# Kernel tuning notes

Hardware: AMD Instinct MI355X
Metric: run time of the kernel (lower is better)

Reference implementation:

```python
import jax, jax.numpy as jnp
import numpy as np
from jax import lax

D_MODEL = 512
EXPAND = 2
INNER = D_MODEL * EXPAND
K = 4
B, T = 8, 2048
LN_EPS = 1e-5


def setup_inputs() -> dict:
    key = jax.random.key(0)
    ks = jax.random.split(key, 12)
    s_in = 1.0 / np.sqrt(D_MODEL)
    s_out = 1.0 / np.sqrt(INNER)
    return {
        "x": jax.random.normal(ks[0], (B, T, D_MODEL), dtype=jnp.float32),
        "ln_w": jnp.ones((D_MODEL,), jnp.float32),
        "ln_b": jnp.zeros((D_MODEL,), jnp.float32),
        "in_proj_w": jax.random.uniform(ks[1], (3 * INNER, D_MODEL), jnp.float32, -s_in, s_in),
        "in_proj_b": jax.random.uniform(ks[2], (3 * INNER,), jnp.float32, -s_in, s_in),
        "conv_w": jax.random.uniform(ks[3], (INNER, 1, K), jnp.float32, -0.5, 0.5),
        "conv_b": jax.random.uniform(ks[4], (INNER,), jnp.float32, -0.5, 0.5),
        "delta_w": jax.random.uniform(ks[5], (INNER, D_MODEL), jnp.float32, -s_in, s_in),
        "delta_b": jax.random.uniform(ks[6], (INNER,), jnp.float32, -s_in, s_in),
        "state_mix": jnp.zeros((INNER,), jnp.float32),
        "skip_scale": jnp.ones((INNER,), jnp.float32),
        "out_proj_w": jax.random.uniform(ks[7], (D_MODEL, INNER), jnp.float32, -s_out, s_out),
        "out_proj_b": jax.random.uniform(ks[8], (D_MODEL,), jnp.float32, -s_out, s_out),
    }


def _layernorm(x, w, b):
    mu = jnp.mean(x, axis=-1, keepdims=True)
    var = jnp.mean(jnp.square(x - mu), axis=-1, keepdims=True)
    return (x - mu) * lax.rsqrt(var + LN_EPS) * w + b


def _causal_dw_conv(x_bct, w, b):
    # x: [B, C, T], w: [C, 1, K] depthwise, left pad K-1 (causal)
    y = lax.conv_general_dilated(
        x_bct, w, window_strides=(1,), padding=[(K - 1, 0)],
        dimension_numbers=("NCH", "OIH", "NCH"), feature_group_count=INNER)
    return y + b[None, :, None]


def reference(x, ln_w, ln_b, in_proj_w, in_proj_b, conv_w, conv_b,
              delta_w, delta_b, state_mix, skip_scale, out_proj_w, out_proj_b):
    residual = x
    xn = _layernorm(x, ln_w, ln_b)                      # [B,T,D]
    h = xn @ in_proj_w.T + in_proj_b                     # [B,T,3*INNER]
    proj, gate, drive = jnp.split(h, 3, axis=-1)
    proj = jax.nn.silu(proj)
    gate = jax.nn.sigmoid(gate)
    conv_out = _causal_dw_conv(jnp.swapaxes(proj, 1, 2), conv_w, conv_b)
    conv_out = jnp.swapaxes(conv_out, 1, 2)              # [B,T,INNER]
    delta = jnp.maximum(jax.nn.sigmoid(xn @ delta_w.T + delta_b), 1e-4)
    drive = jnp.tanh(drive)
    a = jax.nn.sigmoid(state_mix)                        # [INNER]
    d = delta * drive                                    # [B,T,INNER]

    def step(state, d_t):
        state = a * state + d_t
        return state, state

    _, states = lax.scan(step, jnp.zeros((x.shape[0], INNER), x.dtype),
                         jnp.swapaxes(d, 0, 1))          # [T,B,INNER]
    states = jnp.swapaxes(states, 0, 1)                  # [B,T,INNER]
    y = (states + skip_scale * conv_out) * gate
    y = y @ out_proj_w.T + out_proj_b
    return residual + y
```

## Files before the change

kernel.cpp:

```cpp
#include <hip/hip_runtime.h>
#include <stdint.h>

#define D_MODEL 512
#define INNER   1024
#define NCAT    4096
#define BATCH   8
#define SEQ     2048
#define ROWS    (BATCH*SEQ)
#define LN_EPS  1e-5f
#define CHUNK   64
#define NCHUNK  (SEQ/CHUNK)

typedef unsigned short u16;
typedef unsigned int   u32;
typedef __attribute__((ext_vector_type(8))) short bf16x8;
typedef __attribute__((ext_vector_type(4))) float f32x4;

__device__ __forceinline__ u16 f2bf(float f) {
  u32 u = __builtin_bit_cast(u32, f);
  return (u16)((u + 0x7FFFu + ((u >> 16) & 1u)) >> 16);
}
__device__ __forceinline__ float bf2f(u32 lo) {
  return __builtin_bit_cast(float, lo << 16);
}
__device__ __forceinline__ float sigf(float x){ return 1.f/(1.f+__expf(-x)); }

__device__ __forceinline__ void glds16(const void* g, void* l) {
  __builtin_amdgcn_global_load_lds((const __attribute__((address_space(1))) void*)g,
                                   (__attribute__((address_space(3))) void*)l, 16, 0, 0);
}

#define MFMA16(a,b,c) __builtin_amdgcn_mfma_f32_16x16x32_bf16((a),(b),(c),0,0,0)

__global__ __launch_bounds__(256) void ln_kernel(const float* __restrict__ x,
    const float* __restrict__ lw, const float* __restrict__ lb,
    u16* __restrict__ xn) {
  const int row  = blockIdx.x * 4 + (threadIdx.x >> 6);
  const int lane = threadIdx.x & 63;
  const float4* xr = (const float4*)(x + (size_t)row * D_MODEL);
  float4 v0 = xr[lane*2], v1 = xr[lane*2+1];
  float s  = v0.x+v0.y+v0.z+v0.w + v1.x+v1.y+v1.z+v1.w;
  float s2 = v0.x*v0.x+v0.y*v0.y+v0.z*v0.z+v0.w*v0.w
           + v1.x*v1.x+v1.y*v1.y+v1.z*v1.z+v1.w*v1.w;
  #pragma unroll
  for (int o=32;o;o>>=1){ s += __shfl_xor(s,o); s2 += __shfl_xor(s2,o); }
  const float mu = s * (1.f/D_MODEL);
  const float rs = rsqrtf(s2*(1.f/D_MODEL) - mu*mu + LN_EPS);
  const float4* wv = (const float4*)lw; const float4* bv = (const float4*)lb;
  float4 w0 = wv[lane*2], w1 = wv[lane*2+1];
  float4 b0 = bv[lane*2], b1 = bv[lane*2+1];
  u32 p0 = (u32)f2bf((v0.x-mu)*rs*w0.x+b0.x) | ((u32)f2bf((v0.y-mu)*rs*w0.y+b0.y)<<16);
  u32 p1 = (u32)f2bf((v0.z-mu)*rs*w0.z+b0.z) | ((u32)f2bf((v0.w-mu)*rs*w0.w+b0.w)<<16);
  u32 p2 = (u32)f2bf((v1.x-mu)*rs*w1.x+b1.x) | ((u32)f2bf((v1.y-mu)*rs*w1.y+b1.y)<<16);
  u32 p3 = (u32)f2bf((v1.z-mu)*rs*w1.z+b1.z) | ((u32)f2bf((v1.w-mu)*rs*w1.w+b1.w)<<16);
  ((uint4*)(xn + (size_t)row * D_MODEL))[lane] = make_uint4(p0,p1,p2,p3);
}

__global__ __launch_bounds__(256) void cvt_all_kernel(const float* __restrict__ ipw,
    const float* __restrict__ dw, const float* __restrict__ opw,
    const float* __restrict__ ipb, const float* __restrict__ db,
    u16* __restrict__ wcat, u16* __restrict__ wout, float* __restrict__ bcat) {
  const int i = blockIdx.x*256 + threadIdx.x;
  const int NW1 = NCAT*D_MODEL, NW2 = D_MODEL*INNER, STR = gridDim.x*256;
  for (int idx = i; idx < NW1; idx += STR) {
    const int r = idx >> 9, c = idx & 511;
    float v;
    if (r < 2048) v = ipw[idx];
    else {
      const int rr = r - 2048;
      v = (rr & 1) ? dw[(size_t)(rr>>1)*D_MODEL + c]
                   : ipw[(size_t)(2048 + (rr>>1))*D_MODEL + c];
    }
    wcat[idx] = f2bf(v);
  }
  for (int idx = i; idx < NW2; idx += STR) wout[idx] = f2bf(opw[idx]);
  if (i < NCAT) {
    float b;
    if (i < 2048) b = ipb[i];
    else { const int rr = i - 2048; b = (rr & 1) ? db[rr>>1] : ipb[2048 + (rr>>1)]; }
    bcat[i] = b;
  }
}

__device__ __forceinline__ void sched_blk(int nbm, int nbn, int GM, int GN,
                                          int& bM, int& bN) {
  const int nwg = nbm * nbn;
  const int bid = blockIdx.x;
  const int cpx = nwg >> 3;
  const int swz = (bid & 7) * cpx + (bid >> 3);
  const int gsz = GM * GN;
  const int g   = swz / gsz, loc = swz - g * gsz;
  const int ngn = nbn / GN;
  const int gm  = g / ngn,  gn  = g - gm * ngn;
  bM = gm * GM + (loc % GM);
  bN = gn * GN + (loc / GM);
}

__global__ __launch_bounds__(512, 2) void gemm1_kernel(const u16* __restrict__ A,
    const u16* __restrict__ Bm, const float* __restrict__ bcat,
    u16* __restrict__ proj, u16* __restrict__ gate, u16* __restrict__ dbuf) {
  extern __shared__ u16 lds[];
  const int tid = threadIdx.x;
  int bM, bN; sched_blk(ROWS/256, NCAT/256, 8, 4, bM, bN);

  const u16* gA0; const u16* gA1; const u16* gB0; const u16* gB1;
  {
    const int p0 = tid,        q0 = p0>>3, t0 = (p0&7) ^ (q0&7);
    const int p1 = 512 + tid,  q1 = p1>>3, t1 = (p1&7) ^ (q1&7);
    const int rA0 = q0*2 + (t0>>2), sA0 = t0&3;
    const int rA1 = q1*2 + (t1>>2), sA1 = t1&3;
    gA0 = A + (size_t)(bM*256 + rA0)*D_MODEL + sA0*8;
    gA1 = A + (size_t)(bM*256 + rA1)*D_MODEL + sA1*8;
    const int c0 = (rA0 & ~63) + ((rA0&15)*4) + ((rA0>>4)&3);
    const int c1 = (rA1 & ~63) + ((rA1&15)*4) + ((rA1>>4)&3);
    gB0 = Bm + (size_t)(bN*256 + c0)*D_MODEL + sA0*8;
    gB1 = Bm + (size_t)(bN*256 + c1)*D_MODEL + sA1*8;
  }

#define STAGE1(KOFF, BUFO) do { \
    glds16(gA0 + (KOFF), lds + (BUFO) + tid*8); \
    glds16(gA1 + (KOFF), lds + (BUFO) + 4096 + tid*8); \
    glds16(gB0 + (KOFF), lds + (BUFO) + 8192 + tid*8); \
    glds16(gB1 + (KOFF), lds + (BUFO) + 12288 + tid*8); } while(0)

  const int lane = tid & 63, wid = tid >> 6;
  const int wm = wid >> 2, wn = wid & 3;
  const int rl = lane & 15;
  const int e  = (((lane&1)<<2) + (lane>>4)) ^ (rl>>1);
  const int aoff = wm*4096 + (rl>>1)*64 + e*8;
  const int boff = 8192 + wn*2048 + (rl>>1)*64 + e*8;

  f32x4 acc[8][4];
  #pragma unroll
  for (int m=0;m<8;m++)
    #pragma unroll
    for (int n=0;n<4;n++) acc[m][n] = (f32x4){0.f,0.f,0.f,0.f};

  STAGE1(0, 0);
  STAGE1(32, 16384);
  asm volatile("s_waitcnt vmcnt(4)" ::: "memory");
  __builtin_amdgcn_s_barrier();
  __builtin_amdgcn_sched_barrier(0);

  int cur = 0, stg = 32768;
  for (int kt = 0; kt < 16; ++kt) {
    bf16x8 af[8], bfr[4];
    #pragma unroll
    for (int m=0;m<8;m++) af[m]  = *(const bf16x8*)&lds[cur + aoff + m*512];
    #pragma unroll
    for (int n=0;n<4;n++) bfr[n] = *(const bf16x8*)&lds[cur + boff + n*512];
    if (kt + 2 < 16) STAGE1((kt+2)*32, stg);
    #pragma unroll
    for (int m=0;m<8;m++)
      #pragma unroll
      for (int n=0;n<4;n++)
        acc[m][n] = MFMA16(af[m], bfr[n], acc[m][n]);
    if (kt + 2 < 16) { asm volatile("s_waitcnt vmcnt(4)" ::: "memory"); }
    else             { asm volatile("s_waitcnt vmcnt(0)" ::: "memory"); }
    __builtin_amdgcn_s_barrier();
    __builtin_amdgcn_sched_barrier(0);
    cur += 16384; if (cur == 49152) cur = 0;
    stg += 16384; if (stg == 49152) stg = 0;
  }
#undef STAGE1

  const int colb = bN*256 + wn*64 + rl*4;
  const float4 b4 = *(const float4*)&bcat[colb];
  const float* bp = (const float*)&b4;
  if (colb < 2048) {
    u16* outp = (colb < 1024) ? proj : gate;
    const int lcolb = colb & (INNER-1);
    #pragma unroll
    for (int m=0;m<8;m++) {
      const int row0 = bM*256 + wm*128 + m*16 + ((lane>>4)<<2);
      #pragma unroll
      for (int r=0;r<4;r++) {
        float a4[4];
        #pragma unroll
        for (int n=0;n<4;n++) {
          float v = acc[m][n][r] + bp[n];
          a4[n] = (colb < 1024) ? v * sigf(v) : sigf(v);
        }
        u32 lo = (u32)f2bf(a4[0]) | ((u32)f2bf(a4[1])<<16);
        u32 hi = (u32)f2bf(a4[2]) | ((u32)f2bf(a4[3])<<16);
        *(uint2*)&outp[(size_t)(row0+r)*INNER + lcolb] = make_uint2(lo, hi);
      }
    }
  } else {
    const int ch0 = (colb - 2048) >> 1;
    #pragma unroll
    for (int m=0;m<8;m++) {
      const int row0 = bM*256 + wm*128 + m*16 + ((lane>>4)<<2);
      #pragma unroll
      for (int r=0;r<4;r++) {
        const float v0 = acc[m][0][r] + bp[0];
        const float v1 = acc[m][1][r] + bp[1];
        const float v2 = acc[m][2][r] + bp[2];
        const float v3 = acc[m][3][r] + bp[3];
        const float d0 = (2.f*sigf(2.f*v0) - 1.f) * fmaxf(sigf(v1), 1e-4f);
        const float d1 = (2.f*sigf(2.f*v2) - 1.f) * fmaxf(sigf(v3), 1e-4f);
        *(u32*)&dbuf[(size_t)(row0+r)*INNER + ch0] = (u32)f2bf(d0) | ((u32)f2bf(d1)<<16);
      }
    }
  }
}

__device__ __forceinline__ void gemm_main(const u16* __restrict__ A,
    const u16* __restrict__ Bm, int K, int nkt, int bM, int bN,
    u16* lA, u16* lB, f32x4 acc[4][4]) {
  const int tid = threadIdx.x;
  const int l6  = tid >> 2;
  const int sg  = (tid & 3) ^ (l6 & 3);
  const int pB  = (l6 & 15) * 4 + ((l6 >> 4) & 3);
  const u16* gA = A  + (size_t)(bM*128 + l6)*K + sg*8;
  const u16* gB = Bm + (size_t)(bN*128 + pB)*K + sg*8;
  u16* dA = lA + tid*8;
  u16* dB = lB + tid*8;
  const size_t rstep = (size_t)64*K;

#define STAGE_T(koff, bufo) do { \
    const u16* sA = gA + (koff); const u16* sB = gB + (koff); \
    glds16(sA,         dA + (bufo));        glds16(sA + rstep, dA + (bufo) + 2048); \
    glds16(sB,         dB + (bufo));        glds16(sB + rstep, dB + (bufo) + 2048); \
  } while (0)

  STAGE_T(0, 0);
  STAGE_T(32, 4096);
  asm volatile("s_waitcnt vmcnt(4)" ::: "memory");
  __builtin_amdgcn_s_barrier();
  __builtin_amdgcn_sched_barrier(0);

  const int lane = tid & 63, wv = tid >> 6;
  const int wm = wv >> 1, wn = wv & 1;
  const int kx = ((lane>>4) ^ (lane&3)) * 8;
  const int aoff = (wm*64 + (lane&15))*32 + kx;
  const int boff = (wn*64 + (lane&15))*32 + kx;

  int cur = 0, stg = 8192;
  for (int kt = 0; kt < nkt; ++kt) {
    bf16x8 af[4], bfr[4];
    #pragma unroll
    for (int m=0;m<4;m++) af[m]  = *(const bf16x8*)&lA[cur + aoff + m*512];
    #pragma unroll
    for (int n=0;n<4;n++) bfr[n] = *(const bf16x8*)&lB[cur + boff + n*512];
    if (kt + 2 < nkt) STAGE_T((kt+2)*32, stg);
    #pragma unroll
    for (int m=0;m<4;m++)
      #pragma unroll
      for (int n=0;n<4;n++)
        acc[m][n] = MFMA16(af[m], bfr[n], acc[m][n]);
    if (kt + 2 < nkt) { asm volatile("s_waitcnt vmcnt(4)" ::: "memory"); }
    else              { asm volatile("s_waitcnt vmcnt(0)" ::: "memory"); }
    __builtin_amdgcn_s_barrier();
    __builtin_amdgcn_sched_barrier(0);
    cur += 4096; if (cur == 12288) cur = 0;
    stg += 4096; if (stg == 12288) stg = 0;
  }
#undef STAGE_T
}

__global__ __launch_bounds__(256, 3) void gemm2_kernel(const u16* __restrict__ A,
    const u16* __restrict__ Bm, const float* __restrict__ ob,
    const float* __restrict__ resid, float* __restrict__ out) {
  __shared__ u16 lA[12288], lB[12288];
  f32x4 acc[4][4];
  #pragma unroll
  for (int m=0;m<4;m++)
    #pragma unroll
    for (int n=0;n<4;n++) acc[m][n] = (f32x4){0.f,0.f,0.f,0.f};
  int bM, bN; sched_blk(ROWS/128, D_MODEL/128, 8, 4, bM, bN);
  gemm_main(A, Bm, INNER, INNER/32, bM, bN, lA, lB, acc);
  const int lane = threadIdx.x & 63, wv = threadIdx.x >> 6;
  const int wm = wv>>1, wn = wv&1;
  const int colb = bN*128 + wn*64 + (lane&15)*4;
  const float4 ob4 = *(const float4*)&ob[colb];
  #pragma unroll
  for (int m=0;m<4;m++) {
    const int row0 = bM*128 + wm*64 + m*16 + ((lane>>4)<<2);
    #pragma unroll
    for (int r=0;r<4;r++) {
      const size_t idx = (size_t)(row0+r)*D_MODEL + colb;
      float4 rs = *(const float4*)&resid[idx];
      float4 o;
      o.x = acc[m][0][r] + ob4.x + rs.x;
      o.y = acc[m][1][r] + ob4.y + rs.y;
      o.z = acc[m][2][r] + ob4.z + rs.z;
      o.w = acc[m][3][r] + ob4.w + rs.w;
      *(float4*)&out[idx] = o;
    }
  }
}

__global__ __launch_bounds__(256) void scan1_kernel(const u16* __restrict__ d,
    const float* __restrict__ sm, float* __restrict__ cS) {
  const int blk = blockIdx.x;
  const int half = blk & 1, ch = (blk>>1) & (NCHUNK-1), b = blk >> 6;
  const int c0 = half*512 + threadIdx.x*2;
  const float a0 = sigf(sm[c0]), a1 = sigf(sm[c0+1]);
  float s0 = 0.f, s1 = 0.f;
  size_t base = ((size_t)b*SEQ + ch*CHUNK)*INNER + c0;
  for (int t=0;t<CHUNK;t++) {
    u32 du = *(const u32*)(d + base);
    s0 = a0*s0 + bf2f(du & 0xffffu);
    s1 = a1*s1 + bf2f(du >> 16);
    base += INNER;
  }
  const size_t o = ((size_t)b*NCHUNK + ch)*INNER + c0;
  cS[o] = s0; cS[o+1] = s1;
}

__global__ __launch_bounds__(256) void scan2_kernel(const float* __restrict__ sm,
    const float* __restrict__ cS, float* __restrict__ carry) {
  const int idx = blockIdx.x*256 + threadIdx.x;
  const int b = idx >> 9, c0 = (idx & 511)*2;
  const float a0 = sigf(sm[c0]), a1 = sigf(sm[c0+1]);
  float A0 = a0, A1 = a1;
  #pragma unroll
  for (int i=0;i<6;i++){ A0*=A0; A1*=A1; }
  float cr0 = 0.f, cr1 = 0.f;
  for (int ch=0; ch<NCHUNK; ch++) {
    const size_t o = ((size_t)b*NCHUNK + ch)*INNER + c0;
    carry[o] = cr0; carry[o+1] = cr1;
    cr0 = A0*cr0 + cS[o];
    cr1 = A1*cr1 + cS[o+1];
  }
}

__global__ __launch_bounds__(256) void scan3_kernel(const u16* __restrict__ proj,
    const u16* __restrict__ gate, const u16* __restrict__ d,
    const float* __restrict__ carry, const float* __restrict__ sm,
    const float* __restrict__ cw, const float* __restrict__ cb,
    const float* __restrict__ sk, u16* __restrict__ z) {
  const int blk = blockIdx.x;
  const int half = blk & 1, ch = (blk>>1) & (NCHUNK-1), b = blk >> 6;
  const int c0 = half*512 + threadIdx.x*2;
  const float a0 = sigf(sm[c0]), a1 = sigf(sm[c0+1]);
  const float cb0 = cb[c0], cb1 = cb[c0+1];
  const float sk0 = sk[c0], sk1 = sk[c0+1];
  const float w00=cw[c0*4+0], w01=cw[c0*4+1], w02=cw[c0*4+2], w03=cw[c0*4+3];
  const float w10=cw[c0*4+4], w11=cw[c0*4+5], w12=cw[c0*4+6], w13=cw[c0*4+7];
  const size_t o = ((size_t)b*NCHUNK + ch)*INNER + c0;
  float s0 = carry[o], s1 = carry[o+1];
  const int t0 = ch*CHUNK;
  const size_t rowb = (size_t)b*SEQ*INNER + c0;
  float pa0=0,pb0=0,pc0=0, pa1=0,pb1=0,pc1=0;
  if (ch > 0) {
    u32 u3 = *(const u32*)(proj + rowb + (size_t)(t0-3)*INNER);
    u32 u2 = *(const u32*)(proj + rowb + (size_t)(t0-2)*INNER);
    u32 u1 = *(const u32*)(proj + rowb + (size_t)(t0-1)*INNER);
    pa0 = bf2f(u3&0xffffu); pa1 = bf2f(u3>>16);
    pb0 = bf2f(u2&0xffffu); pb1 = bf2f(u2>>16);
    pc0 = bf2f(u1&0xffffu); pc1 = bf2f(u1>>16);
  }
  size_t base = rowb + (size_t)t0*INNER;
  for (int t=0;t<CHUNK;t++) {
    u32 pu = *(const u32*)(proj + base);
    const float pd0 = bf2f(pu&0xffffu), pd1 = bf2f(pu>>16);
    const float co0 = w00*pa0 + w01*pb0 + w02*pc0 + w03*pd0 + cb0;
    const float co1 = w10*pa1 + w11*pb1 + w12*pc1 + w13*pd1 + cb1;
    pa0=pb0; pb0=pc0; pc0=pd0;  pa1=pb1; pb1=pc1; pc1=pd1;
    u32 du = *(const u32*)(d + base);
    s0 = a0*s0 + bf2f(du&0xffffu);
    s1 = a1*s1 + bf2f(du>>16);
    u32 gu = *(const u32*)(gate + base);
    const float z0 = (s0 + sk0*co0)*bf2f(gu&0xffffu);
    const float z1 = (s1 + sk1*co1)*bf2f(gu>>16);
    *(u32*)(z + base) = (u32)f2bf(z0) | ((u32)f2bf(z1)<<16);
    base += INNER;
  }
}

extern "C" void kernel_launch(void* const* d_in, const int* in_sizes, int n_in,
                              void* d_out, int out_size, void* d_ws, size_t ws_size,
                              hipStream_t stream) {
  const float* x    = (const float*)d_in[0];
  const float* ln_w = (const float*)d_in[1];
  const float* ln_b = (const float*)d_in[2];
  const float* ipw  = (const float*)d_in[3];
  const float* ipb  = (const float*)d_in[4];
  const float* cw   = (const float*)d_in[5];
  const float* cb   = (const float*)d_in[6];
  const float* dw   = (const float*)d_in[7];
  const float* db   = (const float*)d_in[8];
  const float* sm   = (const float*)d_in[9];
  const float* sk   = (const float*)d_in[10];
  const float* opw  = (const float*)d_in[11];
  const float* opb  = (const float*)d_in[12];
  float* out = (float*)d_out;

  uint8_t* w = (uint8_t*)d_ws;
  u16* xn    = (u16*)w;  w += (size_t)ROWS*D_MODEL*2;
  u16* wcat  = (u16*)w;  w += (size_t)NCAT*D_MODEL*2;
  u16* wout  = (u16*)w;  w += (size_t)D_MODEL*INNER*2;
  u16* proj  = (u16*)w;  w += (size_t)ROWS*INNER*2;
  u16* gate  = (u16*)w;  w += (size_t)ROWS*INNER*2;
  u16* dbuf  = (u16*)w;  w += (size_t)ROWS*INNER*2;
  u16* z     = (u16*)w;  w += (size_t)ROWS*INNER*2;
  float* cS    = (float*)w; w += (size_t)BATCH*NCHUNK*INNER*4;
  float* carry = (float*)w; w += (size_t)BATCH*NCHUNK*INNER*4;
  float* bcat  = (float*)w; w += (size_t)NCAT*4;

  ln_kernel<<<ROWS/4, 256, 0, stream>>>(x, ln_w, ln_b, xn);
  cvt_all_kernel<<<1024, 256, 0, stream>>>(ipw, dw, opw, ipb, db, wcat, wout, bcat);
  gemm1_kernel<<<(ROWS/256)*(NCAT/256), 512, 98304, stream>>>(xn, wcat, bcat, proj, gate, dbuf);
  scan1_kernel<<<BATCH*NCHUNK*2, 256, 0, stream>>>(dbuf, sm, cS);
  scan2_kernel<<<16, 256, 0, stream>>>(sm, cS, carry);
  scan3_kernel<<<BATCH*NCHUNK*2, 256, 0, stream>>>(proj, gate, dbuf, carry, sm, cw, cb, sk, z);
  gemm2_kernel<<<(ROWS/128)*(D_MODEL/128), 256, 0, stream>>>(z, wout, opb, x, out);
}
```

Baseline: 173.8 us.

## Fuse chunk-local scan reduction into gemm1 epilogue and drop scan1 kernel

The per-chunk state sums of the linear recurrence are now computed inside the gemm1 epilogue. Each lane scans its 4 rows, then wave shuffles with precomputed powers of a combine them into 16-row and then 64-row chunk sums, which are written straight to cS. This removes the scan1 kernel launch and its full re-read of the bf16 drive buffer. In exchange the gemm1 epilogue gets longer and needs more registers, and the chunk sums now use fp32 d values rather than bf16-rounded ones.

```diff
diff --git a/kernel.cpp b/kernel.cpp
--- a/kernel.cpp
+++ b/kernel.cpp
@@ -98,7 +98,8 @@
 
 __global__ __launch_bounds__(512, 2) void gemm1_kernel(const u16* __restrict__ A,
     const u16* __restrict__ Bm, const float* __restrict__ bcat,
-    u16* __restrict__ proj, u16* __restrict__ gate, u16* __restrict__ dbuf) {
+    const float* __restrict__ sm, u16* __restrict__ proj, u16* __restrict__ gate,
+    u16* __restrict__ dbuf, float* __restrict__ cS) {
   extern __shared__ u16 lds[];
   const int tid = threadIdx.x;
   int bM, bN; sched_blk(ROWS/256, NCAT/256, 8, 4, bM, bN);
@@ -188,9 +189,17 @@
     }
   } else {
     const int ch0 = (colb - 2048) >> 1;
+    const int g = lane >> 4;
+    const float A0 = sigf(sm[ch0]), A1 = sigf(sm[ch0+1]);
+    const float A0_2 = A0*A0,   A1_2 = A1*A1;
+    const float A0_4 = A0_2*A0_2, A1_4 = A1_2*A1_2;
+    const float A0_8 = A0_4*A0_4, A1_8 = A1_4*A1_4;
+    const float A0_16 = A0_8*A0_8, A1_16 = A1_8*A1_8;
+    float S0a = 0.f, S0b = 0.f, S1a = 0.f, S1b = 0.f;
     #pragma unroll
     for (int m=0;m<8;m++) {
-      const int row0 = bM*256 + wm*128 + m*16 + ((lane>>4)<<2);
+      const int row0 = bM*256 + wm*128 + m*16 + (g<<2);
+      float sg0 = 0.f, sg1 = 0.f;
       #pragma unroll
       for (int r=0;r<4;r++) {
         const float v0 = acc[m][0][r] + bp[0];
@@ -200,7 +209,25 @@
         const float d0 = (2.f*sigf(2.f*v0) - 1.f) * fmaxf(sigf(v1), 1e-4f);
         const float d1 = (2.f*sigf(2.f*v2) - 1.f) * fmaxf(sigf(v3), 1e-4f);
         *(u32*)&dbuf[(size_t)(row0+r)*INNER + ch0] = (u32)f2bf(d0) | ((u32)f2bf(d1)<<16);
+        sg0 = A0*sg0 + d0;
+        sg1 = A1*sg1 + d1;
       }
+      float p0 = __shfl_xor(sg0, 16), p1 = __shfl_xor(sg1, 16);
+      float e0 = (g & 1) ? (sg0 + A0_4*p0) : (p0 + A0_4*sg0);
+      float e1 = (g & 1) ? (sg1 + A1_4*p1) : (p1 + A1_4*sg1);
+      float q0 = __shfl_xor(e0, 32), q1 = __shfl_xor(e1, 32);
+      float s16_0 = (g & 2) ? (e0 + A0_8*q0) : (q0 + A0_8*e0);
+      float s16_1 = (g & 2) ? (e1 + A1_8*q1) : (q1 + A1_8*e1);
+      if (m < 4) { S0a = A0_16*S0a + s16_0; S1a = A1_16*S1a + s16_1; }
+      else       { S0b = A0_16*S0b + s16_0; S1b = A1_16*S1b + s16_1; }
+    }
+    if (g == 0) {
+      const int b = bM >> 3;
+      const int chunk0 = (bM & 7)*4 + wm*2;
+      const size_t o0 = ((size_t)b*NCHUNK + chunk0    )*INNER + ch0;
+      const size_t o1 = ((size_t)b*NCHUNK + chunk0 + 1)*INNER + ch0;
+      *(float2*)&cS[o0] = make_float2(S0a, S1a);
+      *(float2*)&cS[o1] = make_float2(S0b, S1b);
     }
   }
 }
@@ -289,24 +316,6 @@
       *(float4*)&out[idx] = o;
     }
   }
-}
-
-__global__ __launch_bounds__(256) void scan1_kernel(const u16* __restrict__ d,
-    const float* __restrict__ sm, float* __restrict__ cS) {
-  const int blk = blockIdx.x;
-  const int half = blk & 1, ch = (blk>>1) & (NCHUNK-1), b = blk >> 6;
-  const int c0 = half*512 + threadIdx.x*2;
-  const float a0 = sigf(sm[c0]), a1 = sigf(sm[c0+1]);
-  float s0 = 0.f, s1 = 0.f;
-  size_t base = ((size_t)b*SEQ + ch*CHUNK)*INNER + c0;
-  for (int t=0;t<CHUNK;t++) {
-    u32 du = *(const u32*)(d + base);
-    s0 = a0*s0 + bf2f(du & 0xffffu);
-    s1 = a1*s1 + bf2f(du >> 16);
-    base += INNER;
-  }
-  const size_t o = ((size_t)b*NCHUNK + ch)*INNER + c0;
-  cS[o] = s0; cS[o+1] = s1;
 }
 
 __global__ __launch_bounds__(256) void scan2_kernel(const float* __restrict__ sm,
@@ -402,8 +411,7 @@
 
   ln_kernel<<<ROWS/4, 256, 0, stream>>>(x, ln_w, ln_b, xn);
   cvt_all_kernel<<<1024, 256, 0, stream>>>(ipw, dw, opw, ipb, db, wcat, wout, bcat);
-  gemm1_kernel<<<(ROWS/256)*(NCAT/256), 512, 98304, stream>>>(xn, wcat, bcat, proj, gate, dbuf);
-  scan1_kernel<<<BATCH*NCHUNK*2, 256, 0, stream>>>(dbuf, sm, cS);
+  gemm1_kernel<<<(ROWS/256)*(NCAT/256), 512, 98304, stream>>>(xn, wcat, bcat, sm, proj, gate, dbuf, cS);
   scan2_kernel<<<16, 256, 0, stream>>>(sm, cS, carry);
   scan3_kernel<<<BATCH*NCHUNK*2, 256, 0, stream>>>(proj, gate, dbuf, carry, sm, cw, cb, sk, z);
   gemm2_kernel<<<(ROWS/128)*(D_MODEL/128), 256, 0, stream>>>(z, wout, opb, x, out);
```

New measurement: 168.1 us. 1.03x faster.
